# Kernel optimization log

Measured on AMD Instinct MI355X. Metric: run time of the kernel, lower is better.

## Reference

```python
import jax, jax.numpy as jnp
import numpy as np

B, S, H = 1, 4096, 2048
NH, HD = 16, 128  # num_heads, head_dim = H // NH


def setup_inputs() -> dict:
    key = jax.random.key(0)
    k1, k2, k3 = jax.random.split(key, 3)
    x = jax.random.normal(k1, (B, S, H), dtype=jnp.float32)
    w_qkv = jax.random.normal(k2, (3 * H, H), dtype=jnp.float32) * (1.0 / np.sqrt(H))
    w_out = jax.random.normal(k3, (H, H), dtype=jnp.float32) * (1.0 / np.sqrt(H))
    return {"x": x, "w_qkv": w_qkv, "w_out": w_out}


def reference(x, w_qkv, w_out):
    b, s, _ = x.shape
    # qkv projection: torch Linear computes x @ W^T
    qkv = jnp.einsum('bsh,oh->bso', x, w_qkv)
    qkv = qkv.reshape(b, s, 3, NH, HD).transpose(2, 0, 3, 1, 4)  # [3,B,NH,S,HD]
    q, k, v = qkv[0], qkv[1], qkv[2]
    # world_size == 1 -> single ring step == full attention with online softmax
    scores = jnp.einsum('bhqd,bhkd->bhqk', q, k) / np.sqrt(HD)
    m = jnp.max(scores, axis=-1, keepdims=True)          # running max (single step)
    p = jnp.exp(scores - m)                              # scores_exp
    out = jnp.einsum('bhqk,bhkd->bhqd', p, v)
    denom = jnp.sum(p, axis=-1, keepdims=True) + 1e-8    # running_sum + eps
    out = out / denom
    out = out.transpose(0, 2, 1, 3).reshape(b, s, H)     # [B,S,H]
    return jnp.einsum('bsh,oh->bso', out, w_out)
```

## Files before the change

### kernel.cpp

```cpp
#include <hip/hip_runtime.h>
#include <stdint.h>

typedef __attribute__((ext_vector_type(4))) float f32x4;
typedef __attribute__((ext_vector_type(16))) float f32x16;
typedef __attribute__((ext_vector_type(8))) short bf16x8;
typedef unsigned short u16;

#define MFMA(a, b, c) __builtin_amdgcn_mfma_f32_16x16x32_bf16(a, b, c, 0, 0, 0)
#define MFMA32(a, b, c) __builtin_amdgcn_mfma_f32_32x32x16_bf16(a, b, c, 0, 0, 0)
#define EXP2(x) __builtin_amdgcn_exp2f(x)

__device__ __forceinline__ u16 f2bf(float f) {
  union { float f; unsigned u; } x; x.f = f;
  unsigned r = x.u + 0x7fffu + ((x.u >> 16) & 1u);
  return (u16)(r >> 16);
}

__device__ __forceinline__ unsigned cvtpk(float lo, float hi) {
  unsigned r;
  asm("v_cvt_pk_bf16_f32 %0, %1, %2" : "=v"(r) : "v"(lo), "v"(hi));
  return r;
}

__device__ __forceinline__ void pl32swap(unsigned& a, unsigned& b) {
  asm volatile("v_permlane32_swap_b32 %0, %1" : "+v"(a), "+v"(b));
}

__device__ __forceinline__ void gload16(const void* g, void* l) {
  __builtin_amdgcn_global_load_lds(
      (const __attribute__((address_space(1))) unsigned int*)g,
      (__attribute__((address_space(3))) unsigned int*)l, 16, 0, 0);
}

__global__ void __launch_bounds__(256) cast_bf16(const float* __restrict__ in,
                                                 u16* __restrict__ out, int n4) {
  int i = blockIdx.x * 256 + threadIdx.x;
  if (i >= n4) return;
  float4 v = reinterpret_cast<const float4*>(in)[i];
  ushort4 o;
  o.x = f2bf(v.x); o.y = f2bf(v.y); o.z = f2bf(v.z); o.w = f2bf(v.w);
  reinterpret_cast<ushort4*>(out)[i] = o;
}

template <int EPI>
__global__ void __launch_bounds__(256, 2)
gemm_bt(const u16* __restrict__ A, const u16* __restrict__ B,
        void* __restrict__ C0, void* __restrict__ C1, void* __restrict__ C2,
        int M, int N, int K, int MB) {
  __shared__ alignas(16) u16 sm[8192];
  const int tid = threadIdx.x;
  const int w = tid >> 6, lane = tid & 63;
  const int lr = lane & 15, g = lane >> 4;
  const int mb = blockIdx.x % MB, nb = blockIdx.x / MB;
  const int m0 = mb * 128, n0 = nb * 128;

  const u16* src[4];
  u16* dst[4];
#pragma unroll
  for (int i = 0; i < 4; ++i) {
    int c = w * 4 + i;
    int r = (c & 7) * 16 + (lane >> 2);
    int sb = (lane & 3) ^ ((r >> 1) & 3);
    src[i] = (c < 8) ? (A + (size_t)(m0 + r) * K + sb * 8)
                     : (B + (size_t)(n0 + r) * K + sb * 8);
    dst[i] = &sm[c * 512];
  }

  f32x4 acc[4][4];
#pragma unroll
  for (int x = 0; x < 4; ++x)
#pragma unroll
    for (int y = 0; y < 4; ++y) acc[x][y] = f32x4{0.f, 0.f, 0.f, 0.f};

  const int rowb = (w >> 1) * 64, colb = (w & 1) * 64;
  const int nk = K >> 5;
  for (int kt = 0; kt < nk; ++kt) {
#pragma unroll
    for (int i = 0; i < 4; ++i) gload16(src[i] + kt * 32, dst[i]);
    __syncthreads();
    bf16x8 af[4], bfr[4];
#pragma unroll
    for (int mi = 0; mi < 4; ++mi) {
      int r = rowb + mi * 16 + lr;
      af[mi] = *(const bf16x8*)((const char*)sm + r * 64 +
                                ((g * 16) ^ (((r >> 1) & 3) << 4)));
    }
#pragma unroll
    for (int ni = 0; ni < 4; ++ni) {
      int r = colb + ni * 16 + lr;
      bfr[ni] = *(const bf16x8*)((const char*)sm + 8192 + r * 64 +
                                 ((g * 16) ^ (((r >> 1) & 3) << 4)));
    }
#pragma unroll
    for (int mi = 0; mi < 4; ++mi)
#pragma unroll
      for (int ni = 0; ni < 4; ++ni)
        acc[mi][ni] = MFMA(af[mi], bfr[ni], acc[mi][ni]);
    __syncthreads();
  }

  if (EPI == 0) {
    u16* qo = (u16*)C0;
    u16* ko = (u16*)C1;
    u16* vo = (u16*)C2;
#pragma unroll
    for (int mi = 0; mi < 4; ++mi) {
      int s0 = m0 + rowb + mi * 16 + g * 4;
#pragma unroll
      for (int ni = 0; ni < 4; ++ni) {
        int n = n0 + colb + ni * 16 + lr;
        int t = n >> 11, hh = (n >> 7) & 15, d = n & 127;
        if (t == 2) {
          ushort4 pk;
          pk.x = f2bf(acc[mi][ni][0]);
          pk.y = f2bf(acc[mi][ni][1]);
          pk.z = f2bf(acc[mi][ni][2]);
          pk.w = f2bf(acc[mi][ni][3]);
          *(ushort4*)(vo + (size_t)(hh * 128 + d) * 4096 + s0) = pk;
        } else {
          u16* dq = (t == 0 ? qo : ko) + (size_t)(hh * 4096 + s0) * 128 + d;
#pragma unroll
          for (int j = 0; j < 4; ++j) dq[(size_t)j * 128] = f2bf(acc[mi][ni][j]);
        }
      }
    }
  } else {
    float* C = (float*)C0;
#pragma unroll
    for (int mi = 0; mi < 4; ++mi)
#pragma unroll
      for (int ni = 0; ni < 4; ++ni) {
        size_t r0 = (size_t)(m0 + rowb + mi * 16 + g * 4);
        int cn = n0 + colb + ni * 16 + lr;
#pragma unroll
        for (int j = 0; j < 4; ++j) C[(r0 + j) * N + cn] = acc[mi][ni][j];
      }
  }
}

__global__ void __launch_bounds__(256, 1)
attn_kernel(const u16* __restrict__ qg, const u16* __restrict__ kg,
            const u16* __restrict__ vtg, u16* __restrict__ og) {
  __shared__ alignas(16) u16 sm[32768];
  const int tid = threadIdx.x;
  const int w = tid >> 6, lane = tid & 63;
  const int ql = lane & 31, hl = lane >> 5;
  const int bsw = (blockIdx.x & 7) * 32 + (blockIdx.x >> 3);
  const int h = bsw >> 4;
  const int qb = bsw & 15;

  const u16* ssrc[8];
  u16* sdst[8];
  size_t sstep;
  if (w < 2) {
    sstep = 64 * 128;
#pragma unroll
    for (int i = 0; i < 8; ++i) {
      int c = (w & 1) * 8 + i;
      int r = c * 4 + (lane >> 4);
      int sb = (lane & 15) ^ (r & 7);
      ssrc[i] = kg + (size_t)(h * 4096 + r) * 128 + sb * 8;
      sdst[i] = &sm[c * 512];
    }
  } else {
    sstep = 64;
#pragma unroll
    for (int i = 0; i < 8; ++i) {
      int c = (w & 1) * 8 + i;
      int r = c * 8 + (lane >> 3);
      int sb = (lane & 7) ^ (r & 7);
      ssrc[i] = vtg + (size_t)(h * 128 + r) * 4096 + sb * 8;
      sdst[i] = &sm[16384 + c * 512];
    }
  }

  bf16x8 qf[2][4 * 2];
#pragma unroll
  for (int qc = 0; qc < 2; ++qc) {
    const u16* qrow =
        qg + (size_t)(h * 4096 + qb * 256 + w * 64 + qc * 32 + ql) * 128 + hl * 8;
#pragma unroll
    for (int s = 0; s < 8; ++s) qf[qc][s] = *(const bf16x8*)(qrow + s * 16);
  }

  f32x16 of[2][4];
#pragma unroll
  for (int qc = 0; qc < 2; ++qc)
#pragma unroll
    for (int i = 0; i < 4; ++i)
#pragma unroll
      for (int r = 0; r < 16; ++r) of[qc][i][r] = 0.f;
  float mrun[2] = {-1e30f, -1e30f}, lsum[2] = {0.f, 0.f};
  const float sc2 = 0.08838834764831845f * 1.4426950408889634f;
  const float thr = 6.0f / sc2;

#pragma unroll
  for (int i = 0; i < 8; ++i) gload16(ssrc[i], sdst[i]);

  for (int t = 0; t < 64; ++t) {
    const int cur = t & 1;
    asm volatile("s_waitcnt vmcnt(0)" ::: "memory");
    __builtin_amdgcn_s_barrier();
    asm volatile("" ::: "memory");
    if (t + 1 < 64) {
      const int nb = (t + 1) & 1;
#pragma unroll
      for (int i = 0; i < 8; ++i)
        gload16(ssrc[i] + (size_t)(t + 1) * sstep, sdst[i] + nb * 8192);
    }
    const char* kbuf = (const char*)sm + cur * 16384;
    const char* vbuf = (const char*)sm + 32768 + cur * 16384;

    f32x16 st[2][2];
#pragma unroll
    for (int qc = 0; qc < 2; ++qc)
#pragma unroll
      for (int kb = 0; kb < 2; ++kb)
#pragma unroll
        for (int r = 0; r < 16; ++r) st[qc][kb][r] = 0.f;
    const int swz = (ql & 7) << 4;
#pragma unroll
    for (int s = 0; s < 8; ++s) {
      int off = (s * 32 + hl * 16) ^ swz;
      bf16x8 k0 = *(const bf16x8*)(kbuf + ql * 256 + off);
      bf16x8 k1 = *(const bf16x8*)(kbuf + (32 + ql) * 256 + off);
      st[0][0] = MFMA32(k0, qf[0][s], st[0][0]);
      st[0][1] = MFMA32(k1, qf[0][s], st[0][1]);
      st[1][0] = MFMA32(k0, qf[1][s], st[1][0]);
      st[1][1] = MFMA32(k1, qf[1][s], st[1][1]);
    }

    union U { unsigned u[4]; bf16x8 v; };
    U paf[2][4];
    float esc[2];
#pragma unroll
    for (int qc = 0; qc < 2; ++qc) {
      float tmax = -1e30f;
#pragma unroll
      for (int r = 0; r < 16; ++r)
        tmax = fmaxf(tmax, fmaxf(st[qc][0][r], st[qc][1][r]));
      tmax = fmaxf(tmax, __shfl_xor(tmax, 32));
      float mnew;
      if (__all(tmax - mrun[qc] <= thr)) {
        mnew = mrun[qc];
        esc[qc] = 1.f;
      } else {
        mnew = fmaxf(mrun[qc], tmax);
        esc[qc] = EXP2((mrun[qc] - mnew) * sc2);
#pragma unroll
        for (int db = 0; db < 4; ++db)
#pragma unroll
          for (int r = 0; r < 16; ++r) of[qc][db][r] *= esc[qc];
        mrun[qc] = mnew;
      }
      float mb = mnew * sc2;
      float psum = 0.f;
      unsigned pk0[8], pk1[8];
#pragma unroll
      for (int i = 0; i < 8; ++i) {
        float a0 = EXP2(st[qc][0][2 * i] * sc2 - mb);
        float b0 = EXP2(st[qc][0][2 * i + 1] * sc2 - mb);
        float a1 = EXP2(st[qc][1][2 * i] * sc2 - mb);
        float b1 = EXP2(st[qc][1][2 * i + 1] * sc2 - mb);
        psum += (a0 + b0) + (a1 + b1);
        pk0[i] = cvtpk(a0, b0);
        pk1[i] = cvtpk(a1, b1);
      }
      psum += __shfl_xor(psum, 32);
      lsum[qc] = lsum[qc] * esc[qc] + psum;

      pl32swap(pk0[0], pk0[2]); pl32swap(pk0[1], pk0[3]);
      pl32swap(pk0[4], pk0[6]); pl32swap(pk0[5], pk0[7]);
      pl32swap(pk1[0], pk1[2]); pl32swap(pk1[1], pk1[3]);
      pl32swap(pk1[4], pk1[6]); pl32swap(pk1[5], pk1[7]);
#pragma unroll
      for (int i = 0; i < 4; ++i) {
        paf[qc][0].u[i] = pk0[i];
        paf[qc][1].u[i] = pk0[4 + i];
        paf[qc][2].u[i] = pk1[i];
        paf[qc][3].u[i] = pk1[4 + i];
      }
    }

#pragma unroll
    for (int db = 0; db < 4; ++db) {
      int rr = db * 32 + ql;
      int vswz = (rr & 7) << 4;
#pragma unroll
      for (int kp = 0; kp < 4; ++kp) {
        bf16x8 vf = *(const bf16x8*)(vbuf + rr * 128 + ((kp * 32 + hl * 16) ^ vswz));
        of[0][db] = MFMA32(vf, paf[0][kp].v, of[0][db]);
        of[1][db] = MFMA32(vf, paf[1][kp].v, of[1][db]);
      }
    }
    asm volatile("" ::: "memory");
  }

#pragma unroll
  for (int qc = 0; qc < 2; ++qc) {
    float linv = 1.f / (lsum[qc] + 1e-8f);
    size_t qrow_o =
        (size_t)(qb * 256 + w * 64 + qc * 32 + ql) * 2048 + h * 128;
#pragma unroll
    for (int db = 0; db < 4; ++db)
#pragma unroll
      for (int u = 0; u < 4; ++u) {
        ushort4 pk;
        pk.x = f2bf(of[qc][db][4 * u + 0] * linv);
        pk.y = f2bf(of[qc][db][4 * u + 1] * linv);
        pk.z = f2bf(of[qc][db][4 * u + 2] * linv);
        pk.w = f2bf(of[qc][db][4 * u + 3] * linv);
        *(ushort4*)(og + qrow_o + db * 32 + 8 * u + hl * 4) = pk;
      }
  }
}

extern "C" void kernel_launch(void* const* d_in, const int* in_sizes, int n_in,
                              void* d_out, int out_size, void* d_ws, size_t ws_size,
                              hipStream_t stream) {
  const float* x = (const float*)d_in[0];
  const float* w_qkv = (const float*)d_in[1];
  const float* w_out = (const float*)d_in[2];

  char* ws = (char*)d_ws;
  u16* xb = (u16*)(ws + 0);
  u16* wqkvb = (u16*)(ws + 16777216);
  u16* woutb = (u16*)(ws + 41943040);
  u16* qb = (u16*)(ws + 50331648);
  u16* kb = (u16*)(ws + 67108864);
  u16* vtb = (u16*)(ws + 83886080);
  u16* aob = (u16*)(ws + 100663296);

  cast_bf16<<<8192, 256, 0, stream>>>(x, xb, 2097152);
  cast_bf16<<<12288, 256, 0, stream>>>(w_qkv, wqkvb, 3145728);
  cast_bf16<<<4096, 256, 0, stream>>>(w_out, woutb, 1048576);

  gemm_bt<0><<<32 * 48, 256, 0, stream>>>(xb, wqkvb, qb, kb, vtb, 4096, 6144, 2048, 32);
  attn_kernel<<<256, 256, 0, stream>>>(qb, kb, vtb, aob);
  gemm_bt<1><<<32 * 16, 256, 0, stream>>>(aob, woutb, d_out, nullptr, nullptr, 4096, 2048, 2048, 32);
}
```

Before: 360.9 us.

## Split attention KV range across two wave groups and merge partial softmax results

The attention block doubles to 512 threads. Two groups of four waves each process half of the key/value sequence for the same 256 queries, each group with its own double-buffered LDS tiles. At the end, the second group writes its partial output accumulators and max/sum statistics to shared memory, and the first group merges them with a flash-decoding style rescale before writing bf16 output. This raises the number of waves per CU and halves the serial KV loop length. In exchange it uses about 132KB of LDS and adds a merge step with an extra barrier.

```diff
diff --git a/kernel.cpp b/kernel.cpp
--- a/kernel.cpp
+++ b/kernel.cpp
@@ -138,47 +138,52 @@
   }
 }
 
-__global__ void __launch_bounds__(256, 1)
+__global__ void __launch_bounds__(512, 2)
 attn_kernel(const u16* __restrict__ qg, const u16* __restrict__ kg,
             const u16* __restrict__ vtg, u16* __restrict__ og) {
-  __shared__ alignas(16) u16 sm[32768];
+  __shared__ alignas(16) char smb[135168];
   const int tid = threadIdx.x;
   const int w = tid >> 6, lane = tid & 63;
   const int ql = lane & 31, hl = lane >> 5;
   const int bsw = (blockIdx.x & 7) * 32 + (blockIdx.x >> 3);
   const int h = bsw >> 4;
   const int qb = bsw & 15;
+  const int g2 = w >> 2;
+  const int qw = w & 3;
 
   const u16* ssrc[8];
-  u16* sdst[8];
+  unsigned sdst[8];
   size_t sstep;
-  if (w < 2) {
-    sstep = 64 * 128;
-#pragma unroll
-    for (int i = 0; i < 8; ++i) {
-      int c = (w & 1) * 8 + i;
-      int r = c * 4 + (lane >> 4);
-      int sb = (lane & 15) ^ (r & 7);
-      ssrc[i] = kg + (size_t)(h * 4096 + r) * 128 + sb * 8;
-      sdst[i] = &sm[c * 512];
-    }
-  } else {
-    sstep = 64;
-#pragma unroll
-    for (int i = 0; i < 8; ++i) {
-      int c = (w & 1) * 8 + i;
-      int r = c * 8 + (lane >> 3);
-      int sb = (lane & 7) ^ (r & 7);
-      ssrc[i] = vtg + (size_t)(h * 128 + r) * 4096 + sb * 8;
-      sdst[i] = &sm[16384 + c * 512];
-    }
-  }
-
-  bf16x8 qf[2][4 * 2];
+  {
+    const int sg = w >> 2;
+    if (!(w & 2)) {
+      sstep = 64 * 128;
+#pragma unroll
+      for (int i = 0; i < 8; ++i) {
+        int c = (w & 1) * 8 + i;
+        int r = c * 4 + (lane >> 4);
+        int sb = (lane & 15) ^ (r & 7);
+        ssrc[i] = kg + (size_t)(h * 4096 + sg * 2048 + r) * 128 + sb * 8;
+        sdst[i] = sg * 32768 + c * 1024;
+      }
+    } else {
+      sstep = 64;
+#pragma unroll
+      for (int i = 0; i < 8; ++i) {
+        int c = (w & 1) * 8 + i;
+        int r = c * 8 + (lane >> 3);
+        int sb = (lane & 7) ^ (r & 7);
+        ssrc[i] = vtg + (size_t)(h * 128 + r) * 4096 + sg * 2048 + sb * 8;
+        sdst[i] = 65536 + sg * 32768 + c * 1024;
+      }
+    }
+  }
+
+  bf16x8 qf[2][8];
 #pragma unroll
   for (int qc = 0; qc < 2; ++qc) {
     const u16* qrow =
-        qg + (size_t)(h * 4096 + qb * 256 + w * 64 + qc * 32 + ql) * 128 + hl * 8;
+        qg + (size_t)(h * 4096 + qb * 256 + qw * 64 + qc * 32 + ql) * 128 + hl * 8;
 #pragma unroll
     for (int s = 0; s < 8; ++s) qf[qc][s] = *(const bf16x8*)(qrow + s * 16);
   }
@@ -195,21 +200,21 @@
   const float thr = 6.0f / sc2;
 
 #pragma unroll
-  for (int i = 0; i < 8; ++i) gload16(ssrc[i], sdst[i]);
-
-  for (int t = 0; t < 64; ++t) {
+  for (int i = 0; i < 8; ++i) gload16(ssrc[i], smb + sdst[i]);
+
+  for (int t = 0; t < 32; ++t) {
     const int cur = t & 1;
     asm volatile("s_waitcnt vmcnt(0)" ::: "memory");
     __builtin_amdgcn_s_barrier();
     asm volatile("" ::: "memory");
-    if (t + 1 < 64) {
+    if (t + 1 < 32) {
       const int nb = (t + 1) & 1;
 #pragma unroll
       for (int i = 0; i < 8; ++i)
-        gload16(ssrc[i] + (size_t)(t + 1) * sstep, sdst[i] + nb * 8192);
-    }
-    const char* kbuf = (const char*)sm + cur * 16384;
-    const char* vbuf = (const char*)sm + 32768 + cur * 16384;
+        gload16(ssrc[i] + (size_t)(t + 1) * sstep, smb + sdst[i] + nb * 16384);
+    }
+    const char* kbuf = smb + g2 * 32768 + cur * 16384;
+    const char* vbuf = smb + 65536 + g2 * 32768 + cur * 16384;
 
     f32x16 st[2][2];
 #pragma unroll
@@ -232,7 +237,6 @@
 
     union U { unsigned u[4]; bf16x8 v; };
     U paf[2][4];
-    float esc[2];
 #pragma unroll
     for (int qc = 0; qc < 2; ++qc) {
       float tmax = -1e30f;
@@ -240,17 +244,18 @@
       for (int r = 0; r < 16; ++r)
         tmax = fmaxf(tmax, fmaxf(st[qc][0][r], st[qc][1][r]));
       tmax = fmaxf(tmax, __shfl_xor(tmax, 32));
+      float esc;
       float mnew;
       if (__all(tmax - mrun[qc] <= thr)) {
         mnew = mrun[qc];
-        esc[qc] = 1.f;
+        esc = 1.f;
       } else {
         mnew = fmaxf(mrun[qc], tmax);
-        esc[qc] = EXP2((mrun[qc] - mnew) * sc2);
+        esc = EXP2((mrun[qc] - mnew) * sc2);
 #pragma unroll
         for (int db = 0; db < 4; ++db)
 #pragma unroll
-          for (int r = 0; r < 16; ++r) of[qc][db][r] *= esc[qc];
+          for (int r = 0; r < 16; ++r) of[qc][db][r] *= esc;
         mrun[qc] = mnew;
       }
       float mb = mnew * sc2;
@@ -267,7 +272,7 @@
         pk1[i] = cvtpk(a1, b1);
       }
       psum += __shfl_xor(psum, 32);
-      lsum[qc] = lsum[qc] * esc[qc] + psum;
+      lsum[qc] = lsum[qc] * esc + psum;
 
       pl32swap(pk0[0], pk0[2]); pl32swap(pk0[1], pk0[3]);
       pl32swap(pk0[4], pk0[6]); pl32swap(pk0[5], pk0[7]);
@@ -296,22 +301,47 @@
     asm volatile("" ::: "memory");
   }
 
-#pragma unroll
-  for (int qc = 0; qc < 2; ++qc) {
-    float linv = 1.f / (lsum[qc] + 1e-8f);
-    size_t qrow_o =
-        (size_t)(qb * 256 + w * 64 + qc * 32 + ql) * 2048 + h * 128;
-#pragma unroll
-    for (int db = 0; db < 4; ++db)
-#pragma unroll
-      for (int u = 0; u < 4; ++u) {
-        ushort4 pk;
-        pk.x = f2bf(of[qc][db][4 * u + 0] * linv);
-        pk.y = f2bf(of[qc][db][4 * u + 1] * linv);
-        pk.z = f2bf(of[qc][db][4 * u + 2] * linv);
-        pk.w = f2bf(of[qc][db][4 * u + 3] * linv);
-        *(ushort4*)(og + qrow_o + db * 32 + 8 * u + hl * 4) = pk;
-      }
+  __syncthreads();
+  if (w >= 4) {
+    char* base = smb + qw * 33792 + lane * 512;
+#pragma unroll
+    for (int qc = 0; qc < 2; ++qc)
+#pragma unroll
+      for (int db = 0; db < 4; ++db)
+        *(f32x16*)(base + (qc * 4 + db) * 64) = of[qc][db];
+    float4 ml;
+    ml.x = mrun[0]; ml.y = lsum[0]; ml.z = mrun[1]; ml.w = lsum[1];
+    *(float4*)(smb + qw * 33792 + 32768 + lane * 16) = ml;
+  }
+  __syncthreads();
+  if (w < 4) {
+    const char* base = smb + qw * 33792 + lane * 512;
+    float4 ml = *(const float4*)(smb + qw * 33792 + 32768 + lane * 16);
+#pragma unroll
+    for (int qc = 0; qc < 2; ++qc) {
+      float mo = (qc == 0) ? ml.x : ml.z;
+      float lo = (qc == 0) ? ml.y : ml.w;
+      float m = fmaxf(mrun[qc], mo);
+      float aa = EXP2((mrun[qc] - m) * sc2);
+      float ab = EXP2((mo - m) * sc2);
+      float l = lsum[qc] * aa + lo * ab;
+      float linv = 1.f / (l + 1e-8f);
+      float faa = aa * linv, fab = ab * linv;
+      size_t qrow_o = (size_t)(qb * 256 + qw * 64 + qc * 32 + ql) * 2048 + h * 128;
+#pragma unroll
+      for (int db = 0; db < 4; ++db) {
+        f32x16 ob = *(const f32x16*)(base + (qc * 4 + db) * 64);
+#pragma unroll
+        for (int u = 0; u < 4; ++u) {
+          ushort4 pk;
+          pk.x = f2bf(of[qc][db][4 * u + 0] * faa + ob[4 * u + 0] * fab);
+          pk.y = f2bf(of[qc][db][4 * u + 1] * faa + ob[4 * u + 1] * fab);
+          pk.z = f2bf(of[qc][db][4 * u + 2] * faa + ob[4 * u + 2] * fab);
+          pk.w = f2bf(of[qc][db][4 * u + 3] * faa + ob[4 * u + 3] * fab);
+          *(ushort4*)(og + qrow_o + db * 32 + 8 * u + hl * 4) = pk;
+        }
+      }
+    }
   }
 }
 
@@ -336,6 +366,6 @@
   cast_bf16<<<4096, 256, 0, stream>>>(w_out, woutb, 1048576);
 
   gemm_bt<0><<<32 * 48, 256, 0, stream>>>(xb, wqkvb, qb, kb, vtb, 4096, 6144, 2048, 32);
-  attn_kernel<<<256, 256, 0, stream>>>(qb, kb, vtb, aob);
+  attn_kernel<<<256, 512, 0, stream>>>(qb, kb, vtb, aob);
   gemm_bt<1><<<32 * 16, 256, 0, stream>>>(aob, woutb, d_out, nullptr, nullptr, 4096, 2048, 2048, 32);
 }
```

Result: slower. 502.2 us (+39.1%).
